# Optimization experiments

Measured on AMD Instinct MI355X. Metric: run time of the kernel, lower is better.

Reference implementation:

```python
import jax, jax.numpy as jnp
import numpy as np

B, T, D, H = 4, 2048, 1024, 16
DEPTH = D // H
MASK_NEG = 1e10


def setup_inputs() -> dict:
    key = jax.random.key(0)
    k1, k2, k3 = jax.random.split(key, 3)
    x = jax.random.normal(k1, (B, T, D), dtype=jnp.float32)
    w_attn = jax.random.normal(k2, (D, 3 * D), dtype=jnp.float32) * 0.02
    b_attn = jnp.zeros((3 * D,), dtype=jnp.float32)
    w_proj = jax.random.normal(k3, (D, D), dtype=jnp.float32) * 0.02
    b_proj = jnp.zeros((D,), dtype=jnp.float32)
    return {"x": x, "w_attn": w_attn, "b_attn": b_attn,
            "w_proj": w_proj, "b_proj": b_proj}


def _split_heads(t):
    # (B, T, D) -> (B, H, T, depth)
    return t.reshape(B, T, H, DEPTH).transpose(0, 2, 1, 3)


def reference(x, w_attn, b_attn, w_proj, b_proj):
    # fused QKV projection (GPT-2 conv1d == dense)
    qkv = x @ w_attn + b_attn                      # (B, T, 3D)
    q, k, v = jnp.split(qkv, 3, axis=2)
    q, k, v = _split_heads(q), _split_heads(k), _split_heads(v)
    present = jnp.stack([k, v], axis=1)            # (B, 2, H, T, depth)

    # scaled scores with additive causal mask (as in source: w*b - 1e10*(1-b))
    scores = jnp.einsum('bhqd,bhkd->bhqk', q, k) / jnp.sqrt(
        jnp.asarray(DEPTH, dtype=x.dtype))
    i = jnp.arange(T)[:, None]
    j = jnp.arange(T)[None, :]
    b = (i >= j).astype(scores.dtype)              # (T, T) lower-tri incl diag
    scores = scores * b - MASK_NEG * (1.0 - b)
    attn = jax.nn.softmax(scores, axis=-1)         # (B, H, T, T)

    out = jnp.einsum('bhqk,bhkd->bhqd', attn, v)   # (B, H, T, depth)
    out = out.transpose(0, 2, 1, 3).reshape(B, T, D)
    out = out @ w_proj + b_proj                    # (B, T, D)
    return out, present
```

## Files before the change

kernel.cpp:

```cpp
#include <hip/hip_runtime.h>
#include <hip/hip_bf16.h>
#include <cstdint>
#include <cstddef>

typedef __bf16 y8 __attribute__((ext_vector_type(8)));
typedef float f4 __attribute__((ext_vector_type(4)));
typedef unsigned short u16t;

#define NB 4
#define TT 2048
#define DD 1024
#define HH 16

static constexpr size_t OUT0 = (size_t)NB * TT * DD;
#define QSCALE 0.180336880111120426f

__device__ __forceinline__ u16t bf16r(float f) {
    union { float f; unsigned u; } x; x.f = f;
    return (u16t)((x.u + 0x7FFFu + ((x.u >> 16) & 1u)) >> 16);
}

__device__ __forceinline__ unsigned cvtpk(float lo, float hi) {
    unsigned r;
    asm("v_cvt_pk_bf16_f32 %0, %1, %2" : "=v"(r) : "v"(lo), "v"(hi));
    return r;
}

#define GLDS16(g, s) __builtin_amdgcn_global_load_lds( \
    (__attribute__((address_space(1))) void*)(g),      \
    (__attribute__((address_space(3))) void*)(s), 16, 0, 0)

#define BARX() asm volatile("s_barrier" ::: "memory")
#define VMW(n) asm volatile("s_waitcnt vmcnt(" #n ")" ::: "memory")
#define LGKM0() asm volatile("s_waitcnt lgkmcnt(0)" ::: "memory")

__global__ __launch_bounds__(256)
void cvt_f32_bf16(const float* __restrict__ in, u16t* __restrict__ outp, int n) {
    int i = (blockIdx.x * 256 + threadIdx.x) * 8;
    if (i >= n) return;
    float4 a = *(const float4*)(in + i);
    float4 b = *(const float4*)(in + i + 4);
    union { u16t h[8]; uint4 q; } u;
    u.h[0] = bf16r(a.x); u.h[1] = bf16r(a.y); u.h[2] = bf16r(a.z); u.h[3] = bf16r(a.w);
    u.h[4] = bf16r(b.x); u.h[5] = bf16r(b.y); u.h[6] = bf16r(b.z); u.h[7] = bf16r(b.w);
    *(uint4*)(outp + i) = u.q;
}

__global__ __launch_bounds__(256)
void transpose_w(const float* __restrict__ in, u16t* __restrict__ outp, int Kd, int Nd,
                 int qlim, float qs) {
    __shared__ float tile[32][33];
    const int n0 = blockIdx.x * 32, k0 = blockIdx.y * 32;
    const int tx = threadIdx.x & 31, ty = threadIdx.x >> 5;
    for (int yy = ty; yy < 32; yy += 8)
        tile[yy][tx] = in[(size_t)(k0 + yy) * Nd + n0 + tx];
    __syncthreads();
    for (int yy = ty; yy < 32; yy += 8) {
        float v = tile[tx][yy];
        if (n0 + yy < qlim) v *= qs;
        outp[(size_t)(n0 + yy) * Kd + k0 + tx] = bf16r(v);
    }
}

template<int MODE, int TPB>
__global__ __launch_bounds__(256, 2)
void gemm_bt(const u16t* __restrict__ A, const u16t* __restrict__ Bt,
             const float* __restrict__ bias, float* __restrict__ C,
             float* __restrict__ pres, u16t* __restrict__ qb,
             u16t* __restrict__ kb, u16t* __restrict__ vtb,
             int N, int K)
{
    __shared__ u16t ldsA[2][128 * 64];
    __shared__ u16t ldsB[2][128 * 64];
    const int tid = threadIdx.x;
    const int w = tid >> 6, l = tid & 63;
    const int wr = w >> 1, wc = w & 1;
    const int lr = l & 15, lq = l >> 4;

    auto stage = [&](int bm, int bn, int k0, int pi) {
#pragma unroll
        for (int c = 0; c < 4; ++c) {
            const int L = ((w * 64 + l) << 4) + (c << 12);
            const int row = L >> 7;
            const int col = (((L >> 4) & 7) ^ (row & 7)) << 3;
            GLDS16(A + (size_t)(bm + row) * K + k0 + col,
                   (char*)ldsA[pi] + (w << 10) + (c << 12));
            GLDS16(Bt + (size_t)(bn + row) * K + k0 + col,
                   (char*)ldsB[pi] + (w << 10) + (c << 12));
        }
    };

    const int nt = K >> 6;

#pragma unroll
    for (int j = 0; j < TPB; ++j) {
        const int idx = blockIdx.x * TPB + j;
        const int bm = (idx & 63) << 7;
        const int bn = (idx >> 6) << 7;

        f4 acc[4][4] = {};
        if (j == 0) stage(bm, bn, 0, 0);

        for (int t = 0; t < nt; ++t) {
            if (t + 1 < nt) { stage(bm, bn, (t + 1) << 6, (t + 1) & 1); VMW(8); }
            else            { VMW(0); }
            BARX();
            const char* La = (const char*)ldsA[t & 1];
            const char* Lb = (const char*)ldsB[t & 1];
#pragma unroll
            for (int ks = 0; ks < 2; ++ks) {
                y8 af[4], bfv[4];
#pragma unroll
                for (int m = 0; m < 4; ++m) {
                    const int row = wr * 64 + m * 16 + lr;
                    const int slot = (lq + ks * 4) ^ (row & 7);
                    af[m] = *(const y8*)(La + row * 128 + (slot << 4));
                }
#pragma unroll
                for (int n = 0; n < 4; ++n) {
                    const int row = wc * 64 + n * 16 + lr;
                    const int slot = (lq + ks * 4) ^ (row & 7);
                    bfv[n] = *(const y8*)(Lb + row * 128 + (slot << 4));
                }
#pragma unroll
                for (int m = 0; m < 4; ++m)
#pragma unroll
                    for (int n = 0; n < 4; ++n)
                        acc[m][n] = __builtin_amdgcn_mfma_f32_16x16x32_bf16(af[m], bfv[n], acc[m][n], 0, 0, 0);
            }
            BARX();
        }

        if (j + 1 < TPB) {
            const int nx = idx + 1;
            stage((nx & 63) << 7, (nx >> 6) << 7, 0, 0);
        }

        if (MODE == 0) {
#pragma unroll
            for (int m = 0; m < 4; ++m) {
                const int rowb = bm + wr * 64 + m * 16 + 4 * lq;
#pragma unroll
                for (int n = 0; n < 4; ++n) {
                    const int col = bn + wc * 64 + n * 16 + lr;
                    const float bv = bias[col];
#pragma unroll
                    for (int r = 0; r < 4; ++r)
                        C[(size_t)(rowb + r) * N + col] = acc[m][n][r] + bv;
                }
            }
        } else {
            const int part = bn >> 10;

            if (part == 2) {
#pragma unroll
                for (int m = 0; m < 4; ++m) {
                    const int rowb = bm + wr * 64 + m * 16 + 4 * lq;
                    const int b0 = rowb >> 11, t0 = rowb & 2047;
#pragma unroll
                    for (int n = 0; n < 4; ++n) {
                        const int colg = bn + wc * 64 + n * 16 + lr;
                        const float bv = bias[colg];
                        const int cl = colg & 1023;
                        const int h = cl >> 6, d = cl & 63;
                        uint2 pk;
                        pk.x = cvtpk(acc[m][n][0] + bv, acc[m][n][1] + bv);
                        pk.y = cvtpk(acc[m][n][2] + bv, acc[m][n][3] + bv);
                        *(uint2*)(vtb + ((size_t)(b0 * HH + h) * 64 + d) * TT + t0) = pk;
                    }
                }
            }

            {
                char* const half = wr ? (char*)ldsB[1] : (char*)ldsA[1];
#pragma unroll
                for (int m = 0; m < 4; ++m)
#pragma unroll
                    for (int n = 0; n < 4; ++n) {
                        const int co = wc * 64 + n * 16 + lr;
                        float bv = bias[bn + co];
                        if (part == 0) bv *= QSCALE;
#pragma unroll
                        for (int r = 0; r < 4; ++r) {
                            const int ro = m * 16 + 4 * lq + r;
                            *(u16t*)(half + ro * 256 + ((((co >> 3) ^ (ro & 7))) << 4)
                                     + ((co & 7) << 1)) = bf16r(acc[m][n][r] + bv);
                        }
                    }
            }
            LGKM0();
            BARX();

            const int hb = (bn & 1023) >> 6;
#pragma unroll
            for (int s = 0; s < 8; ++s) {
                const int sr = s >> 1, sc = s & 1;
                const int row = sr * 32 + w * 8 + (l >> 3);
                const char* rh = (row & 64) ? (const char*)ldsB[1] : (const char*)ldsA[1];
                const int ro = row & 63;
                const int c = sc * 8 + (l & 7);
                union { y8 v; uint4 q; u16t h[8]; } u;
                u.v = *(const y8*)(rh + ro * 256 + ((c ^ (ro & 7)) << 4));
                const int tglob = bm + row;
                const int b0 = tglob >> 11, tt = tglob & 2047;
                const int h2 = hb + sc;
                const int d0 = (c & 7) * 8;
                const size_t base = (((size_t)(b0 * HH + h2)) * TT + tt) * 64 + d0;
                if (part == 0) {
                    *(uint4*)(qb + base) = u.q;
                } else {
                    if (part == 1) *(uint4*)(kb + base) = u.q;
                    float4 f0, f1;
                    f0.x = __uint_as_float((unsigned)u.h[0] << 16);
                    f0.y = __uint_as_float((unsigned)u.h[1] << 16);
                    f0.z = __uint_as_float((unsigned)u.h[2] << 16);
                    f0.w = __uint_as_float((unsigned)u.h[3] << 16);
                    f1.x = __uint_as_float((unsigned)u.h[4] << 16);
                    f1.y = __uint_as_float((unsigned)u.h[5] << 16);
                    f1.z = __uint_as_float((unsigned)u.h[6] << 16);
                    f1.w = __uint_as_float((unsigned)u.h[7] << 16);
                    const size_t pb = OUT0 +
                        (((size_t)((b0 * 2 + (part - 1)) * HH + h2)) * TT + tt) * 64 + d0;
                    *(float4*)(pres + pb) = f0;
                    *(float4*)(pres + pb + 4) = f1;
                }
            }
            BARX();
        }
    }
}

__global__ __launch_bounds__(256, 2)
void attn_fwd(const u16t* __restrict__ qg, const u16t* __restrict__ kg,
              const u16t* __restrict__ vtg, u16t* __restrict__ og)
{
    __shared__ u16t sQ[128 * 64];
    __shared__ u16t sK[2 * 64 * 64];
    __shared__ u16t sV[2 * 64 * 64];
    __shared__ u16t sP[4 * 32 * 64];
    const int tid = threadIdx.x;
    const int w = tid >> 6, l = tid & 63;
    const int lr = l & 15, lq = l >> 4;
    const int qt = 15 - blockIdx.y;
    const int bh = blockIdx.x;
    const int b = bh >> 4, h = bh & 15;
    const u16t* qsrc = qg + (size_t)bh * TT * 64;
    const u16t* ksrc = kg + (size_t)bh * TT * 64;
    const u16t* vsrc = vtg + (size_t)bh * 64 * TT;

    auto stageKV = [&](int kt, int pi) {
        const int kv0 = kt << 6;
#pragma unroll
        for (int c = 0; c < 2; ++c) {
            const int L = ((w * 64 + l) << 4) + (c << 12);
            const int row = L >> 7;
            const int col = (((L >> 4) & 7) ^ (row & 7)) << 3;
            GLDS16(ksrc + (kv0 + row) * 64 + col,
                   (char*)sK + (pi << 13) + (w << 10) + (c << 12));
            GLDS16(vsrc + (size_t)row * TT + kv0 + col,
                   (char*)sV + (pi << 13) + (w << 10) + (c << 12));
        }
    };

#pragma unroll
    for (int c = 0; c < 4; ++c) {
        const int L = ((w * 64 + l) << 4) + (c << 12);
        const int row = L >> 7;
        const int col = (((L >> 4) & 7) ^ (row & 7)) << 3;
        GLDS16(qsrc + (qt * 128 + row) * 64 + col, (char*)sQ + (w << 10) + (c << 12));
    }
    stageKV(0, 0);
    __syncthreads();

    y8 qf[2][2];
#pragma unroll
    for (int qm = 0; qm < 2; ++qm)
#pragma unroll
        for (int ks = 0; ks < 2; ++ks) {
            const int row = w * 32 + qm * 16 + lr;
            const int slot = (lq + ks * 4) ^ (row & 7);
            qf[qm][ks] = *(const y8*)((const char*)sQ + row * 128 + (slot << 4));
        }

    f4 o[2][4] = {};
    float mrow[2] = {-1e30f, -1e30f};
    float lsum[2] = {0.f, 0.f};

    char* Pw = (char*)sP + (w << 12);
    const int qmax = qt * 128 + w * 32 + 31;
    const int ktiles = 2 * qt + 2;
    int cur = 0;

    for (int kt = 0; kt < ktiles; ++kt) {
        __syncthreads();
        if (kt + 1 < ktiles) stageKV(kt + 1, cur ^ 1);
        const int kv0 = kt << 6;
        if (kv0 <= qmax) {
            const char* Kb = (const char*)sK + (cur << 13);
            const char* Vb = (const char*)sV + (cur << 13);

            f4 s[2][4] = {};
            __builtin_amdgcn_s_setprio(1);
#pragma unroll
            for (int ks = 0; ks < 2; ++ks) {
                y8 kf[4];
#pragma unroll
                for (int n = 0; n < 4; ++n) {
                    const int row = n * 16 + lr;
                    const int slot = (lq + ks * 4) ^ (row & 7);
                    kf[n] = *(const y8*)(Kb + row * 128 + (slot << 4));
                }
#pragma unroll
                for (int qm = 0; qm < 2; ++qm)
#pragma unroll
                    for (int n = 0; n < 4; ++n)
                        s[qm][n] = __builtin_amdgcn_mfma_f32_16x16x32_bf16(kf[n], qf[qm][ks], s[qm][n], 0, 0, 0);
            }
            __builtin_amdgcn_s_setprio(0);

#pragma unroll
            for (int qm = 0; qm < 2; ++qm) {
                const int qb0 = qt * 128 + w * 32 + qm * 16;
                if (kv0 + 63 > qb0) {
                    const int query = qb0 + lr;
#pragma unroll
                    for (int n = 0; n < 4; ++n)
#pragma unroll
                        for (int r = 0; r < 4; ++r)
                            if (kv0 + n * 16 + 4 * lq + r > query) s[qm][n][r] = -1e30f;
                }

                float mx = -1e30f;
#pragma unroll
                for (int n = 0; n < 4; ++n)
                    mx = fmaxf(mx, fmaxf(fmaxf(s[qm][n][0], s[qm][n][1]),
                                         fmaxf(s[qm][n][2], s[qm][n][3])));
                mx = fmaxf(mx, __shfl_xor(mx, 16));
                mx = fmaxf(mx, __shfl_xor(mx, 32));

                if (!__all(mx <= mrow[qm] + 8.f)) {
                    const float newm = fmaxf(mrow[qm], mx);
                    const float corr = exp2f(mrow[qm] - newm);
                    mrow[qm] = newm;
                    lsum[qm] *= corr;
#pragma unroll
                    for (int n = 0; n < 4; ++n) o[qm][n] *= corr;
                }

                float rs = 0.f;
#pragma unroll
                for (int n = 0; n < 4; ++n)
#pragma unroll
                    for (int r = 0; r < 4; ++r) {
                        const float p = exp2f(s[qm][n][r] - mrow[qm]);
                        s[qm][n][r] = p;
                        rs += p;
                    }
                lsum[qm] += rs;

                const int prow = qm * 16 + lr;
                const int rbase = prow * 128 + ((lq & 1) << 3);
#pragma unroll
                for (int n = 0; n < 4; ++n) {
                    uint2 pk;
                    pk.x = cvtpk(s[qm][n][0], s[qm][n][1]);
                    pk.y = cvtpk(s[qm][n][2], s[qm][n][3]);
                    const int sIdx = 2 * n + (lq >> 1);
                    *(uint2*)(Pw + rbase + ((sIdx ^ (prow & 7)) << 4)) = pk;
                }
            }

            __builtin_amdgcn_s_setprio(1);
#pragma unroll
            for (int ks = 0; ks < 2; ++ks) {
                y8 vf[4], pf[2];
#pragma unroll
                for (int n = 0; n < 4; ++n) {
                    const int row = n * 16 + lr;
                    const int slot = (lq + ks * 4) ^ (row & 7);
                    vf[n] = *(const y8*)(Vb + row * 128 + (slot << 4));
                }
#pragma unroll
                for (int qm = 0; qm < 2; ++qm) {
                    const int row = qm * 16 + lr;
                    const int slot = (lq + ks * 4) ^ (row & 7);
                    pf[qm] = *(const y8*)(Pw + row * 128 + (slot << 4));
                }
#pragma unroll
                for (int qm = 0; qm < 2; ++qm)
#pragma unroll
                    for (int n = 0; n < 4; ++n)
                        o[qm][n] = __builtin_amdgcn_mfma_f32_16x16x32_bf16(vf[n], pf[qm], o[qm][n], 0, 0, 0);
            }
            __builtin_amdgcn_s_setprio(0);
        }
        cur ^= 1;
    }

#pragma unroll
    for (int qm = 0; qm < 2; ++qm) {
        float t = lsum[qm];
        t += __shfl_xor(t, 16);
        t += __shfl_xor(t, 32);
        const float inv = 1.0f / t;
        const int trow = qt * 128 + w * 32 + qm * 16 + lr;
#pragma unroll
        for (int n = 0; n < 4; ++n) {
            uint2 pk;
            pk.x = cvtpk(o[qm][n][0] * inv, o[qm][n][1] * inv);
            pk.y = cvtpk(o[qm][n][2] * inv, o[qm][n][3] * inv);
            *(uint2*)(og + ((size_t)(b * TT + trow)) * DD + h * 64 + n * 16 + 4 * lq) = pk;
        }
    }
}

extern "C" void kernel_launch(void* const* d_in, const int* in_sizes, int n_in,
                              void* d_out, int out_size, void* d_ws, size_t ws_size,
                              hipStream_t stream) {
    const float* x      = (const float*)d_in[0];
    const float* w_attn = (const float*)d_in[1];
    const float* b_attn = (const float*)d_in[2];
    const float* w_proj = (const float*)d_in[3];
    const float* b_proj = (const float*)d_in[4];
    float* outp = (float*)d_out;
    char* ws = (char*)d_ws;

    u16t* xb  = (u16t*)(ws + 0);
    u16t* wta = (u16t*)(ws + 16777216);
    u16t* wtp = (u16t*)(ws + 23068672);
    u16t* qb  = (u16t*)(ws + 25165824);
    u16t* kb  = (u16t*)(ws + 41943040);
    u16t* vtb = (u16t*)(ws + 58720256);
    if (ws_size < 75497472) return;

    cvt_f32_bf16<<<4096, 256, 0, stream>>>(x, xb, 8388608);
    transpose_w<<<dim3(96, 32), 256, 0, stream>>>(w_attn, wta, 1024, 3072, 1024, QSCALE);
    transpose_w<<<dim3(32, 32), 256, 0, stream>>>(w_proj, wtp, 1024, 1024, 0, 1.0f);

    gemm_bt<1, 3><<<512, 256, 0, stream>>>(xb, wta, b_attn, nullptr, outp,
                                           qb, kb, vtb, 3072, 1024);
    attn_fwd<<<dim3(64, 16), 256, 0, stream>>>(qb, kb, vtb, xb );
    gemm_bt<0, 1><<<512, 256, 0, stream>>>(xb, wtp, b_proj, outp,
                                           nullptr, nullptr, nullptr, nullptr,
                                           1024, 1024);
}
```

Before: 197.5 us.

## Switch GEMMs to 256x128 tiles with 512-thread blocks, drop persistent multi-tile loop

The GEMM kernel now uses 8 waves per block computing a 256x128 output tile, with the A tile shared across twice as many rows of waves. The earlier persistent scheme, where each block walked 3 tiles in sequence, is replaced by one tile per block. The QKV GEMM launches 768 blocks and the projection GEMM 256. This is meant to raise B-tile reuse and cut global load traffic per FLOP. In exchange it uses 96KB of LDS per block and allows only one block per CU, and the 256-block projection launch may leave compute units idle.

```diff
diff --git a/kernel.cpp b/kernel.cpp
--- a/kernel.cpp
+++ b/kernel.cpp
@@ -62,170 +62,161 @@
     }
 }
 
-template<int MODE, int TPB>
-__global__ __launch_bounds__(256, 2)
+template<int MODE>
+__global__ __launch_bounds__(512, 1)
 void gemm_bt(const u16t* __restrict__ A, const u16t* __restrict__ Bt,
              const float* __restrict__ bias, float* __restrict__ C,
              float* __restrict__ pres, u16t* __restrict__ qb,
              u16t* __restrict__ kb, u16t* __restrict__ vtb,
              int N, int K)
 {
-    __shared__ u16t ldsA[2][128 * 64];
-    __shared__ u16t ldsB[2][128 * 64];
+    __shared__ char sm[98304];
+    char* const smA0 = sm;
+    char* const smB0 = sm + 65536;
     const int tid = threadIdx.x;
     const int w = tid >> 6, l = tid & 63;
     const int wr = w >> 1, wc = w & 1;
     const int lr = l & 15, lq = l >> 4;
-
-    auto stage = [&](int bm, int bn, int k0, int pi) {
+    const int idx = blockIdx.x;
+    const int bm = (idx & 31) << 8;
+    const int bn = (idx >> 5) << 7;
+
+    auto stage = [&](int k0, int pi) {
 #pragma unroll
         for (int c = 0; c < 4; ++c) {
-            const int L = ((w * 64 + l) << 4) + (c << 12);
+            const int L = (tid << 4) + (c << 13);
             const int row = L >> 7;
             const int col = (((L >> 4) & 7) ^ (row & 7)) << 3;
             GLDS16(A + (size_t)(bm + row) * K + k0 + col,
-                   (char*)ldsA[pi] + (w << 10) + (c << 12));
+                   smA0 + (pi << 15) + (tid << 4) + (c << 13));
+        }
+#pragma unroll
+        for (int c = 0; c < 2; ++c) {
+            const int L = (tid << 4) + (c << 13);
+            const int row = L >> 7;
+            const int col = (((L >> 4) & 7) ^ (row & 7)) << 3;
             GLDS16(Bt + (size_t)(bn + row) * K + k0 + col,
-                   (char*)ldsB[pi] + (w << 10) + (c << 12));
+                   smB0 + (pi << 14) + (tid << 4) + (c << 13));
         }
     };
 
+    f4 acc[4][4] = {};
     const int nt = K >> 6;
 
-#pragma unroll
-    for (int j = 0; j < TPB; ++j) {
-        const int idx = blockIdx.x * TPB + j;
-        const int bm = (idx & 63) << 7;
-        const int bn = (idx >> 6) << 7;
-
-        f4 acc[4][4] = {};
-        if (j == 0) stage(bm, bn, 0, 0);
-
-        for (int t = 0; t < nt; ++t) {
-            if (t + 1 < nt) { stage(bm, bn, (t + 1) << 6, (t + 1) & 1); VMW(8); }
-            else            { VMW(0); }
-            BARX();
-            const char* La = (const char*)ldsA[t & 1];
-            const char* Lb = (const char*)ldsB[t & 1];
-#pragma unroll
-            for (int ks = 0; ks < 2; ++ks) {
-                y8 af[4], bfv[4];
-#pragma unroll
-                for (int m = 0; m < 4; ++m) {
-                    const int row = wr * 64 + m * 16 + lr;
-                    const int slot = (lq + ks * 4) ^ (row & 7);
-                    af[m] = *(const y8*)(La + row * 128 + (slot << 4));
-                }
-#pragma unroll
-                for (int n = 0; n < 4; ++n) {
-                    const int row = wc * 64 + n * 16 + lr;
-                    const int slot = (lq + ks * 4) ^ (row & 7);
-                    bfv[n] = *(const y8*)(Lb + row * 128 + (slot << 4));
-                }
-#pragma unroll
-                for (int m = 0; m < 4; ++m)
-#pragma unroll
-                    for (int n = 0; n < 4; ++n)
-                        acc[m][n] = __builtin_amdgcn_mfma_f32_16x16x32_bf16(af[m], bfv[n], acc[m][n], 0, 0, 0);
-            }
-            BARX();
-        }
-
-        if (j + 1 < TPB) {
-            const int nx = idx + 1;
-            stage((nx & 63) << 7, (nx >> 6) << 7, 0, 0);
-        }
-
-        if (MODE == 0) {
+    stage(0, 0);
+    for (int t = 0; t < nt; ++t) {
+        if (t + 1 < nt) { stage((t + 1) << 6, (t + 1) & 1); VMW(6); }
+        else            { VMW(0); }
+        BARX();
+        const char* La = smA0 + ((t & 1) << 15);
+        const char* Lb = smB0 + ((t & 1) << 14);
+#pragma unroll
+        for (int ks = 0; ks < 2; ++ks) {
+            y8 af[4], bfv[4];
+#pragma unroll
+            for (int m = 0; m < 4; ++m) {
+                const int row = wr * 64 + m * 16 + lr;
+                const int slot = (lq + ks * 4) ^ (row & 7);
+                af[m] = *(const y8*)(La + row * 128 + (slot << 4));
+            }
+#pragma unroll
+            for (int n = 0; n < 4; ++n) {
+                const int row = wc * 64 + n * 16 + lr;
+                const int slot = (lq + ks * 4) ^ (row & 7);
+                bfv[n] = *(const y8*)(Lb + row * 128 + (slot << 4));
+            }
+#pragma unroll
+            for (int m = 0; m < 4; ++m)
+#pragma unroll
+                for (int n = 0; n < 4; ++n)
+                    acc[m][n] = __builtin_amdgcn_mfma_f32_16x16x32_bf16(af[m], bfv[n], acc[m][n], 0, 0, 0);
+        }
+        BARX();
+    }
+
+    if (MODE == 0) {
+#pragma unroll
+        for (int m = 0; m < 4; ++m) {
+            const int rowb = bm + wr * 64 + m * 16 + 4 * lq;
+#pragma unroll
+            for (int n = 0; n < 4; ++n) {
+                const int col = bn + wc * 64 + n * 16 + lr;
+                const float bv = bias[col];
+#pragma unroll
+                for (int r = 0; r < 4; ++r)
+                    C[(size_t)(rowb + r) * N + col] = acc[m][n][r] + bv;
+            }
+        }
+    } else {
+        const int part = bn >> 10;
+
+        if (part == 2) {
 #pragma unroll
             for (int m = 0; m < 4; ++m) {
                 const int rowb = bm + wr * 64 + m * 16 + 4 * lq;
+                const int b0 = rowb >> 11, t0 = rowb & 2047;
 #pragma unroll
                 for (int n = 0; n < 4; ++n) {
-                    const int col = bn + wc * 64 + n * 16 + lr;
-                    const float bv = bias[col];
-#pragma unroll
-                    for (int r = 0; r < 4; ++r)
-                        C[(size_t)(rowb + r) * N + col] = acc[m][n][r] + bv;
-                }
-            }
-        } else {
-            const int part = bn >> 10;
-
-            if (part == 2) {
-#pragma unroll
-                for (int m = 0; m < 4; ++m) {
-                    const int rowb = bm + wr * 64 + m * 16 + 4 * lq;
-                    const int b0 = rowb >> 11, t0 = rowb & 2047;
-#pragma unroll
-                    for (int n = 0; n < 4; ++n) {
-                        const int colg = bn + wc * 64 + n * 16 + lr;
-                        const float bv = bias[colg];
-                        const int cl = colg & 1023;
-                        const int h = cl >> 6, d = cl & 63;
-                        uint2 pk;
-                        pk.x = cvtpk(acc[m][n][0] + bv, acc[m][n][1] + bv);
-                        pk.y = cvtpk(acc[m][n][2] + bv, acc[m][n][3] + bv);
-                        *(uint2*)(vtb + ((size_t)(b0 * HH + h) * 64 + d) * TT + t0) = pk;
-                    }
-                }
-            }
-
-            {
-                char* const half = wr ? (char*)ldsB[1] : (char*)ldsA[1];
-#pragma unroll
-                for (int m = 0; m < 4; ++m)
-#pragma unroll
-                    for (int n = 0; n < 4; ++n) {
-                        const int co = wc * 64 + n * 16 + lr;
-                        float bv = bias[bn + co];
-                        if (part == 0) bv *= QSCALE;
-#pragma unroll
-                        for (int r = 0; r < 4; ++r) {
-                            const int ro = m * 16 + 4 * lq + r;
-                            *(u16t*)(half + ro * 256 + ((((co >> 3) ^ (ro & 7))) << 4)
-                                     + ((co & 7) << 1)) = bf16r(acc[m][n][r] + bv);
-                        }
-                    }
-            }
-            LGKM0();
-            BARX();
-
-            const int hb = (bn & 1023) >> 6;
-#pragma unroll
-            for (int s = 0; s < 8; ++s) {
-                const int sr = s >> 1, sc = s & 1;
-                const int row = sr * 32 + w * 8 + (l >> 3);
-                const char* rh = (row & 64) ? (const char*)ldsB[1] : (const char*)ldsA[1];
-                const int ro = row & 63;
-                const int c = sc * 8 + (l & 7);
-                union { y8 v; uint4 q; u16t h[8]; } u;
-                u.v = *(const y8*)(rh + ro * 256 + ((c ^ (ro & 7)) << 4));
-                const int tglob = bm + row;
-                const int b0 = tglob >> 11, tt = tglob & 2047;
-                const int h2 = hb + sc;
-                const int d0 = (c & 7) * 8;
-                const size_t base = (((size_t)(b0 * HH + h2)) * TT + tt) * 64 + d0;
-                if (part == 0) {
-                    *(uint4*)(qb + base) = u.q;
-                } else {
-                    if (part == 1) *(uint4*)(kb + base) = u.q;
-                    float4 f0, f1;
-                    f0.x = __uint_as_float((unsigned)u.h[0] << 16);
-                    f0.y = __uint_as_float((unsigned)u.h[1] << 16);
-                    f0.z = __uint_as_float((unsigned)u.h[2] << 16);
-                    f0.w = __uint_as_float((unsigned)u.h[3] << 16);
-                    f1.x = __uint_as_float((unsigned)u.h[4] << 16);
-                    f1.y = __uint_as_float((unsigned)u.h[5] << 16);
-                    f1.z = __uint_as_float((unsigned)u.h[6] << 16);
-                    f1.w = __uint_as_float((unsigned)u.h[7] << 16);
-                    const size_t pb = OUT0 +
-                        (((size_t)((b0 * 2 + (part - 1)) * HH + h2)) * TT + tt) * 64 + d0;
-                    *(float4*)(pres + pb) = f0;
-                    *(float4*)(pres + pb + 4) = f1;
-                }
-            }
-            BARX();
+                    const int colg = bn + wc * 64 + n * 16 + lr;
+                    const float bv = bias[colg];
+                    const int cl = colg & 1023;
+                    const int h = cl >> 6, d = cl & 63;
+                    uint2 pk;
+                    pk.x = cvtpk(acc[m][n][0] + bv, acc[m][n][1] + bv);
+                    pk.y = cvtpk(acc[m][n][2] + bv, acc[m][n][3] + bv);
+                    *(uint2*)(vtb + ((size_t)(b0 * HH + h) * 64 + d) * TT + t0) = pk;
+                }
+            }
+        }
+
+#pragma unroll
+        for (int m = 0; m < 4; ++m)
+#pragma unroll
+            for (int n = 0; n < 4; ++n) {
+                const int co = wc * 64 + n * 16 + lr;
+                float bv = bias[bn + co];
+                if (part == 0) bv *= QSCALE;
+#pragma unroll
+                for (int r = 0; r < 4; ++r) {
+                    const int ro = wr * 64 + m * 16 + 4 * lq + r;
+                    *(u16t*)(smA0 + ro * 256 + (((co >> 3) ^ (ro & 7)) << 4)
+                             + ((co & 7) << 1)) = bf16r(acc[m][n][r] + bv);
+                }
+            }
+        LGKM0();
+        BARX();
+
+        const int hb = (bn & 1023) >> 6;
+        const int c = tid & 15;
+        const int rw = tid >> 4;
+        const int h2 = hb + (c >> 3);
+        const int d0 = (c & 7) * 8;
+#pragma unroll
+        for (int s = 0; s < 8; ++s) {
+            const int row = s * 32 + rw;
+            union { y8 v; uint4 q; u16t h[8]; } u;
+            u.v = *(const y8*)(smA0 + row * 256 + ((c ^ (row & 7)) << 4));
+            const int tglob = bm + row;
+            const int b0 = tglob >> 11, tt = tglob & 2047;
+            const size_t base = (((size_t)(b0 * HH + h2)) * TT + tt) * 64 + d0;
+            if (part == 0) {
+                *(uint4*)(qb + base) = u.q;
+            } else {
+                if (part == 1) *(uint4*)(kb + base) = u.q;
+                float4 f0, f1;
+                f0.x = __uint_as_float((unsigned)u.h[0] << 16);
+                f0.y = __uint_as_float((unsigned)u.h[1] << 16);
+                f0.z = __uint_as_float((unsigned)u.h[2] << 16);
+                f0.w = __uint_as_float((unsigned)u.h[3] << 16);
+                f1.x = __uint_as_float((unsigned)u.h[4] << 16);
+                f1.y = __uint_as_float((unsigned)u.h[5] << 16);
+                f1.z = __uint_as_float((unsigned)u.h[6] << 16);
+                f1.w = __uint_as_float((unsigned)u.h[7] << 16);
+                const size_t pb = OUT0 +
+                    (((size_t)((b0 * 2 + (part - 1)) * HH + h2)) * TT + tt) * 64 + d0;
+                *(float4*)(pres + pb) = f0;
+                *(float4*)(pres + pb + 4) = f1;
+            }
         }
     }
 }
@@ -437,10 +428,10 @@
     transpose_w<<<dim3(96, 32), 256, 0, stream>>>(w_attn, wta, 1024, 3072, 1024, QSCALE);
     transpose_w<<<dim3(32, 32), 256, 0, stream>>>(w_proj, wtp, 1024, 1024, 0, 1.0f);
 
-    gemm_bt<1, 3><<<512, 256, 0, stream>>>(xb, wta, b_attn, nullptr, outp,
-                                           qb, kb, vtb, 3072, 1024);
+    gemm_bt<1><<<768, 512, 0, stream>>>(xb, wta, b_attn, nullptr, outp,
+                                        qb, kb, vtb, 3072, 1024);
     attn_fwd<<<dim3(64, 16), 256, 0, stream>>>(qb, kb, vtb, xb );
-    gemm_bt<0, 1><<<512, 256, 0, stream>>>(xb, wtp, b_proj, outp,
-                                           nullptr, nullptr, nullptr, nullptr,
-                                           1024, 1024);
-}
+    gemm_bt<0><<<256, 512, 0, stream>>>(xb, wtp, b_proj, outp,
+                                        nullptr, nullptr, nullptr, nullptr,
+                                        1024, 1024);
+}
```

Measured after the change: 193.0 us. 1.02x faster.
